# Optimization experiments

Measured on AMD Instinct MI355X. Metric: run time of the kernel, lower is better.

The kernel has to match this reference:

```python
import jax, jax.numpy as jnp
import numpy as np


def _squash(t, axis):
    # matches torch: t / norm * (norm^2 / (1 + norm^2))
    ns = jnp.sum(t * t, axis=axis, keepdims=True)
    norm = jnp.sqrt(ns)
    return t / norm * (ns / (1.0 + ns))


def setup_inputs() -> dict:
    key = jax.random.key(0)
    k1, k2 = jax.random.split(key)
    B, I, A_IN, O, A_OUT = 16, 2048, 16, 64, 32
    x = jax.random.normal(k1, (B, I, A_IN, 1), dtype=jnp.float32)
    # nn.init.normal(std=0.1)
    weights = jax.random.normal(k2, (I, A_IN, O * A_OUT), dtype=jnp.float32) * 0.1
    # nn.init.constant(val=0.1)
    bias = jnp.full((O, A_OUT), 0.1, dtype=jnp.float32)
    return {"x": x, "weights": weights, "bias": bias}


def reference(x, weights, bias):
    B = x.shape[0]
    I, A_IN, OA = weights.shape
    O, A = bias.shape
    NUM_ROUTING = 3  # hardcoded in the torch forward

    # votes = sum over input_atoms of broadcast(x) * weights  -> [B, I, O, A]
    votes = jnp.einsum('bia,iaj->bij', x[..., 0], weights).reshape(B, I, O, A)
    votes_sg = jax.lax.stop_gradient(votes)

    logits = jnp.zeros((B, I, O), dtype=votes.dtype)
    activation = None
    for i in range(NUM_ROUTING):
        route = jax.nn.softmax(logits, axis=2)  # over output_dim
        v = votes if i == NUM_ROUTING - 1 else votes_sg
        # weighted sum over input capsules: [B, O, A]
        preactivate = jnp.einsum('bio,bioa->boa', route, v) + bias
        activation = _squash(preactivate, axis=2)
        if i < NUM_ROUTING - 1:
            # agreement between votes and current output capsules
            distances = jnp.einsum('bioa,boa->bio', votes, activation)
            logits = logits + distances
    return activation
```

## Files before the change

### kernel.cpp

```cpp
#include <hip/hip_runtime.h>
#include <math.h>

#define B_   16
#define I_   2048
#define AIN_ 16
#define O_   64
#define J_   2048
#define JP_  1024

__device__ __forceinline__ unsigned bf16rne(float f) {
  unsigned u = __float_as_uint(f);
  return (u + 0x7FFFu + ((u >> 16) & 1u)) >> 16;
}
__device__ __forceinline__ float bf16lo(unsigned p) { return __uint_as_float(p << 16); }
__device__ __forceinline__ float bf16hi(unsigned p) { return __uint_as_float(p & 0xFFFF0000u); }

__device__ __forceinline__ float2 ntload2(const float2* p) {
  union { double d; float2 f; } u;
  u.d = __builtin_nontemporal_load((const double*)p);
  return u.f;
}

__global__ __launch_bounds__(512) void votes_kernel(
    const float* __restrict__ x, const float* __restrict__ W,
    unsigned* __restrict__ votes)
{
  __shared__ float x_lds[4 * B_ * AIN_];
  const int tid = threadIdx.x;
  const int islab = blockIdx.x >> 1, jt = blockIdx.x & 1;
  const int i0 = islab * 4;

  for (int e = tid; e < 4 * B_ * AIN_; e += 512) {
    int b = e >> 5 & 15, il = e >> 9, a = e & 15;
    il = e >> 8; b = (e >> 4) & 15; a = e & 15;
    x_lds[il * 256 + b * 16 + a] =
        x[(size_t)b * (I_ * AIN_) + (size_t)(i0 + il) * AIN_ + a];
  }
  __syncthreads();

  const float2* __restrict__ Wq = (const float2*)W;
  const int jp = jt * 512 + tid;

  for (int il = 0; il < 4; ++il) {
    const int i = i0 + il;
    const float2* __restrict__ Wi = Wq + (size_t)i * (AIN_ * JP_) + jp;
    const float2* __restrict__ xq = (const float2*)x_lds + il * 128;

    float2 v[16];
    #pragma unroll
    for (int b = 0; b < 16; ++b) v[b] = make_float2(0.f, 0.f);

    #pragma unroll
    for (int a2 = 0; a2 < 8; ++a2) {
      float2 w0 = ntload2(Wi + (size_t)(2 * a2 + 0) * JP_);
      float2 w1 = ntload2(Wi + (size_t)(2 * a2 + 1) * JP_);
      #pragma unroll
      for (int b = 0; b < 16; ++b) {
        float2 xv = xq[b * 8 + a2];
        v[b].x = fmaf(xv.x, w0.x, v[b].x);
        v[b].y = fmaf(xv.x, w0.y, v[b].y);
        v[b].x = fmaf(xv.y, w1.x, v[b].x);
        v[b].y = fmaf(xv.y, w1.y, v[b].y);
      }
    }

    unsigned* __restrict__ vo = votes + (size_t)i * (B_ * JP_) + jp;
    #pragma unroll
    for (int b = 0; b < 16; ++b)
      vo[(size_t)b * JP_] = bf16rne(v[b].x) | (bf16rne(v[b].y) << 16);
  }
}

__global__ __launch_bounds__(256) void reduce0_kernel(
    const uint4* __restrict__ votes4, const float* __restrict__ bias,
    float* __restrict__ act)
{
  __shared__ float red[64][4][8];
  const int b = blockIdx.x >> 6, o = blockIdx.x & 63;
  const int t = threadIdx.x, s = t >> 2, q = t & 3;
  const uint4* __restrict__ vp = votes4 + (size_t)b * 256 + (size_t)(o * 4 + q);

  float a0=0.f,a1=0.f,a2=0.f,a3=0.f,a4=0.f,a5=0.f,a6=0.f,a7=0.f;
  #pragma unroll 8
  for (int k = 0; k < 32; ++k) {
    uint4 u = vp[(size_t)(s + 64 * k) * 4096];
    a0 += bf16lo(u.x); a1 += bf16hi(u.x);
    a2 += bf16lo(u.y); a3 += bf16hi(u.y);
    a4 += bf16lo(u.z); a5 += bf16hi(u.z);
    a6 += bf16lo(u.w); a7 += bf16hi(u.w);
  }
  red[s][q][0]=a0; red[s][q][1]=a1; red[s][q][2]=a2; red[s][q][3]=a3;
  red[s][q][4]=a4; red[s][q][5]=a5; red[s][q][6]=a6; red[s][q][7]=a7;
  __syncthreads();

  if (t < 32) {
    const int q2 = t >> 3, e = t & 7;
    float p = 0.f;
    for (int s2 = 0; s2 < 64; ++s2) p += red[s2][q2][e];
    p = p * (1.0f / 64.0f) + bias[o * 32 + q2 * 8 + e];
    float ns = p * p;
    ns += __shfl_xor(ns, 1);  ns += __shfl_xor(ns, 2);
    ns += __shfl_xor(ns, 4);  ns += __shfl_xor(ns, 8);
    ns += __shfl_xor(ns, 16);
    act[(size_t)b * J_ + o * 32 + q2 * 8 + e] = p * sqrtf(ns) / (1.0f + ns);
  }
}

template<int PASS>
__global__ __launch_bounds__(256) void route_kernel(
    const uint4* __restrict__ votes4, const float* __restrict__ act_in,
    float* __restrict__ part, float* __restrict__ logits)
{
  __shared__ float d_lds[128];
  __shared__ float r_lds[128];

  const int t = threadIdx.x;
  const int islab = blockIdx.x >> 3, bq = blockIdx.x & 7;
  const int i0 = islab * 8;
  const int o = t >> 2, l4 = t & 3;
  const float4* __restrict__ actq = (const float4*)act_in;

  float4 av00 = actq[(size_t)(bq * 2 + 0) * 512 + 2 * t];
  float4 av01 = actq[(size_t)(bq * 2 + 0) * 512 + 2 * t + 1];
  float4 av10 = actq[(size_t)(bq * 2 + 1) * 512 + 2 * t];
  float4 av11 = actq[(size_t)(bq * 2 + 1) * 512 + 2 * t + 1];

  float4 ac00 = make_float4(0,0,0,0), ac01 = make_float4(0,0,0,0);
  float4 ac10 = make_float4(0,0,0,0), ac11 = make_float4(0,0,0,0);

  for (int il = 0; il < 8; ++il) {
    const int i = i0 + il;
    float lgv = 0.f;
    if (PASS == 2 && t < 128)
      lgv = logits[((size_t)(bq * 2 + (t >> 6)) * I_ + i) * O_ + (t & 63)];

    const uint4* __restrict__ vo =
        votes4 + (size_t)i * 4096 + (size_t)(bq * 2) * 256 + t;
    uint4 v0 = vo[0];
    uint4 v1 = vo[256];

    float c0 = bf16lo(v0.x)*av00.x + bf16hi(v0.x)*av00.y
             + bf16lo(v0.y)*av00.z + bf16hi(v0.y)*av00.w
             + bf16lo(v0.z)*av01.x + bf16hi(v0.z)*av01.y
             + bf16lo(v0.w)*av01.z + bf16hi(v0.w)*av01.w;
    c0 += __shfl_xor(c0, 1);  c0 += __shfl_xor(c0, 2);
    float c1 = bf16lo(v1.x)*av10.x + bf16hi(v1.x)*av10.y
             + bf16lo(v1.y)*av10.z + bf16hi(v1.y)*av10.w
             + bf16lo(v1.z)*av11.x + bf16hi(v1.z)*av11.y
             + bf16lo(v1.w)*av11.z + bf16hi(v1.w)*av11.w;
    c1 += __shfl_xor(c1, 1);  c1 += __shfl_xor(c1, 2);
    if (l4 == 0) d_lds[o]      = c0;
    if (l4 == 1) d_lds[64 + o] = c1;
    __syncthreads();

    float ellsave = 0.f;
    if (t < 128) {
      float ell = d_lds[t];
      if (PASS == 2) ell += lgv;
      ellsave = ell;
      float m = ell;
      m = fmaxf(m, __shfl_xor(m, 32)); m = fmaxf(m, __shfl_xor(m, 16));
      m = fmaxf(m, __shfl_xor(m, 8));  m = fmaxf(m, __shfl_xor(m, 4));
      m = fmaxf(m, __shfl_xor(m, 2));  m = fmaxf(m, __shfl_xor(m, 1));
      float e = __expf(ell - m);
      float sd = e;
      sd += __shfl_xor(sd, 32); sd += __shfl_xor(sd, 16); sd += __shfl_xor(sd, 8);
      sd += __shfl_xor(sd, 4);  sd += __shfl_xor(sd, 2);  sd += __shfl_xor(sd, 1);
      r_lds[t] = e / sd;
    }
    __syncthreads();

    if (PASS == 1 && t < 128)
      logits[((size_t)(bq * 2 + (t >> 6)) * I_ + i) * O_ + (t & 63)] = ellsave;

    float r0 = r_lds[o], r1 = r_lds[64 + o];
    ac00.x = fmaf(r0, bf16lo(v0.x), ac00.x); ac00.y = fmaf(r0, bf16hi(v0.x), ac00.y);
    ac00.z = fmaf(r0, bf16lo(v0.y), ac00.z); ac00.w = fmaf(r0, bf16hi(v0.y), ac00.w);
    ac01.x = fmaf(r0, bf16lo(v0.z), ac01.x); ac01.y = fmaf(r0, bf16hi(v0.z), ac01.y);
    ac01.z = fmaf(r0, bf16lo(v0.w), ac01.z); ac01.w = fmaf(r0, bf16hi(v0.w), ac01.w);
    ac10.x = fmaf(r1, bf16lo(v1.x), ac10.x); ac10.y = fmaf(r1, bf16hi(v1.x), ac10.y);
    ac10.z = fmaf(r1, bf16lo(v1.y), ac10.z); ac10.w = fmaf(r1, bf16hi(v1.y), ac10.w);
    ac11.x = fmaf(r1, bf16lo(v1.z), ac11.x); ac11.y = fmaf(r1, bf16hi(v1.z), ac11.y);
    ac11.z = fmaf(r1, bf16lo(v1.w), ac11.z); ac11.w = fmaf(r1, bf16hi(v1.w), ac11.w);
  }

  float4* __restrict__ po =
      (float4*)part + (size_t)islab * 8192 + (size_t)(bq * 2) * 512 + 2 * t;
  po[0]   = ac00;  po[1]   = ac01;
  po[512] = ac10;  po[513] = ac11;
}

__global__ __launch_bounds__(256) void reduce_squash(
    const float* __restrict__ part, const float* __restrict__ bias,
    float* __restrict__ out)
{
  __shared__ float4 red[32][8];
  const int b = blockIdx.x >> 6, o = blockIdx.x & 63;
  const int t = threadIdx.x, s = t >> 3, q = t & 7;
  const float4* __restrict__ base =
      (const float4*)part + (size_t)b * 512 + o * 8 + q;

  float4 acc = make_float4(0.f, 0.f, 0.f, 0.f);
  #pragma unroll
  for (int k = 0; k < 8; ++k) {
    float4 v = base[(size_t)(s + 32 * k) * 8192];
    acc.x += v.x; acc.y += v.y; acc.z += v.z; acc.w += v.w;
  }
  red[s][q] = acc;
  __syncthreads();

  if (t < 8) {
    float4 p = make_float4(0.f, 0.f, 0.f, 0.f);
    for (int s2 = 0; s2 < 32; ++s2) {
      float4 v = red[s2][t];
      p.x += v.x; p.y += v.y; p.z += v.z; p.w += v.w;
    }
    float4 bq4 = ((const float4*)bias)[o * 8 + t];
    p.x += bq4.x; p.y += bq4.y; p.z += bq4.z; p.w += bq4.w;
    float ns = p.x*p.x + p.y*p.y + p.z*p.z + p.w*p.w;
    ns += __shfl_xor(ns, 1);  ns += __shfl_xor(ns, 2);  ns += __shfl_xor(ns, 4);
    float sc = sqrtf(ns) / (1.0f + ns);
    ((float4*)out)[(size_t)b * 512 + o * 8 + t] =
        make_float4(p.x*sc, p.y*sc, p.z*sc, p.w*sc);
  }
}

template<int PASS>
__global__ __launch_bounds__(1024) void fb_pass_kernel(
    const float* __restrict__ x, const float* __restrict__ W,
    const float* __restrict__ act_in, float* __restrict__ part,
    float* __restrict__ logits)
{
  __shared__ float x_lds[8 * B_ * AIN_];
  __shared__ float d_lds[8 * O_];
  __shared__ float r_lds[8 * O_];
  const int tid = threadIdx.x, blk = blockIdx.x, i0 = blk * 8;
  for (int e = tid; e < 8 * B_ * AIN_; e += 1024) {
    int b = e >> 7, il = (e >> 4) & 7, a = e & 15;
    x_lds[il * 256 + b * 16 + a] =
        x[(size_t)b * (I_ * AIN_) + (size_t)(i0 + il) * AIN_ + a];
  }
  __syncthreads();
  const int og = tid >> 4, lg = tid & 15;
  float2 acc[16];
  #pragma unroll
  for (int b = 0; b < 16; ++b) acc[b] = make_float2(0.f, 0.f);
  const float2* __restrict__ Wq   = (const float2*)W;
  const float2* __restrict__ actq = (const float2*)act_in;
  for (int il = 0; il < 8; ++il) {
    const int i = i0 + il;
    const float2* __restrict__ Wi = Wq + (size_t)i * (AIN_ * JP_);
    const float4* __restrict__ xq = (const float4*)x_lds + il * 64;
    for (int h = 0; h < 2; ++h) {
      float2 v[8];
      #pragma unroll
      for (int bb = 0; bb < 8; ++bb) v[bb] = make_float2(0.f, 0.f);
      #pragma unroll
      for (int a4 = 0; a4 < 4; ++a4) {
        float2 w0 = Wi[(size_t)(a4 * 4 + 0) * JP_ + tid];
        float2 w1 = Wi[(size_t)(a4 * 4 + 1) * JP_ + tid];
        float2 w2 = Wi[(size_t)(a4 * 4 + 2) * JP_ + tid];
        float2 w3 = Wi[(size_t)(a4 * 4 + 3) * JP_ + tid];
        #pragma unroll
        for (int bb = 0; bb < 8; ++bb) {
          float4 xv = xq[(h * 8 + bb) * 4 + a4];
          v[bb].x = fmaf(xv.x, w0.x, v[bb].x); v[bb].y = fmaf(xv.x, w0.y, v[bb].y);
          v[bb].x = fmaf(xv.y, w1.x, v[bb].x); v[bb].y = fmaf(xv.y, w1.y, v[bb].y);
          v[bb].x = fmaf(xv.z, w2.x, v[bb].x); v[bb].y = fmaf(xv.z, w2.y, v[bb].y);
          v[bb].x = fmaf(xv.w, w3.x, v[bb].x); v[bb].y = fmaf(xv.w, w3.y, v[bb].y);
        }
      }
      if (PASS == 0) {
        #pragma unroll
        for (int bb = 0; bb < 8; ++bb) {
          acc[h * 8 + bb].x += v[bb].x; acc[h * 8 + bb].y += v[bb].y;
        }
      } else {
        #pragma unroll
        for (int bb = 0; bb < 8; ++bb) {
          const int b = h * 8 + bb;
          float2 avv = actq[(size_t)b * JP_ + tid];
          float c = v[bb].x * avv.x + v[bb].y * avv.y;
          c += __shfl_xor(c, 1); c += __shfl_xor(c, 2);
          c += __shfl_xor(c, 4); c += __shfl_xor(c, 8);
          if (lg == bb) d_lds[bb * 64 + og] = c;
        }
        __syncthreads();
        if (tid < 512) {
          const int bb2 = tid >> 6, o2 = tid & 63;
          const int b2  = h * 8 + bb2;
          float ell = d_lds[tid];
          if (PASS == 2) ell += logits[((size_t)b2 * I_ + i) * O_ + o2];
          if (PASS == 1) logits[((size_t)b2 * I_ + i) * O_ + o2] = ell;
          float m = ell;
          m = fmaxf(m, __shfl_xor(m, 32)); m = fmaxf(m, __shfl_xor(m, 16));
          m = fmaxf(m, __shfl_xor(m, 8));  m = fmaxf(m, __shfl_xor(m, 4));
          m = fmaxf(m, __shfl_xor(m, 2));  m = fmaxf(m, __shfl_xor(m, 1));
          float e = __expf(ell - m);
          float s = e;
          s += __shfl_xor(s, 32); s += __shfl_xor(s, 16); s += __shfl_xor(s, 8);
          s += __shfl_xor(s, 4);  s += __shfl_xor(s, 2);  s += __shfl_xor(s, 1);
          r_lds[tid] = e / s;
        }
        __syncthreads();
        #pragma unroll
        for (int bb = 0; bb < 8; ++bb) {
          float r = r_lds[bb * 64 + og];
          acc[h * 8 + bb].x = fmaf(r, v[bb].x, acc[h * 8 + bb].x);
          acc[h * 8 + bb].y = fmaf(r, v[bb].y, acc[h * 8 + bb].y);
        }
      }
    }
  }
  const float sc = (PASS == 0) ? (1.0f / 64.0f) : 1.0f;
  #pragma unroll
  for (int b = 0; b < 16; ++b) {
    float2* __restrict__ po = (float2*)part +
        (size_t)blk * (B_ * JP_) + (size_t)b * JP_ + tid;
    *po = make_float2(acc[b].x * sc, acc[b].y * sc);
  }
}

extern "C" void kernel_launch(void* const* d_in, const int* in_sizes, int n_in,
                              void* d_out, int out_size, void* d_ws, size_t ws_size,
                              hipStream_t stream) {
  const float* x    = (const float*)d_in[0];
  const float* W    = (const float*)d_in[1];
  const float* bias = (const float*)d_in[2];
  float* out = (float*)d_out;

  float*    part   = (float*)d_ws;
  float*    act    = part + (size_t)256 * (B_ * J_);
  float*    logits = act + (B_ * J_);
  unsigned* votes  = (unsigned*)(logits + (size_t)B_ * I_ * O_);
  const size_t need = ((size_t)256 * B_ * J_ + B_ * J_ + (size_t)B_ * I_ * O_) * 4
                    + (size_t)I_ * B_ * JP_ * 4;

  if (ws_size >= need) {
    votes_kernel<<<1024, 512, 0, stream>>>(x, W, votes);
    reduce0_kernel<<<1024, 256, 0, stream>>>((const uint4*)votes, bias, act);
    route_kernel<1><<<2048, 256, 0, stream>>>((const uint4*)votes, act, part, logits);
    reduce_squash<<<1024, 256, 0, stream>>>(part, bias, act);
    route_kernel<2><<<2048, 256, 0, stream>>>((const uint4*)votes, act, part, logits);
    reduce_squash<<<1024, 256, 0, stream>>>(part, bias, out);
  } else {
    fb_pass_kernel<0><<<256, 1024, 0, stream>>>(x, W, act, part, logits);
    reduce_squash<<<1024, 256, 0, stream>>>(part, bias, act);
    fb_pass_kernel<1><<<256, 1024, 0, stream>>>(x, W, act, part, logits);
    reduce_squash<<<1024, 256, 0, stream>>>(part, bias, act);
    fb_pass_kernel<2><<<256, 1024, 0, stream>>>(x, W, act, part, logits);
    reduce_squash<<<1024, 256, 0, stream>>>(part, bias, out);
  }
}
```

Measured before the change: 190.5 us.

## Fuse first routing pass partial sums into votes kernel

The votes kernel now also accumulates fp32 partial sums of the votes over its 8-row input slab and writes them to a partials buffer, scaled by the uniform first-pass route weight of 1/64. A new reduce kernel sums these partials and applies bias and squash, so the full bf16 votes tensor no longer has to be re-read for the first routing pass. Blocks change to 256 threads covering 8 input rows each, with a waves-per-EU attribute. The first-pass sums now come from fp32 values rather than bf16-rounded ones, and the reduce contains some redundant arithmetic on p.x.

```diff
diff --git a/kernel.cpp b/kernel.cpp
--- a/kernel.cpp
+++ b/kernel.cpp
@@ -21,27 +21,32 @@
   return u.f;
 }
 
-__global__ __launch_bounds__(512) void votes_kernel(
+__global__ __launch_bounds__(256)
+__attribute__((amdgpu_waves_per_eu(4, 4)))
+void votes_p0_kernel(
     const float* __restrict__ x, const float* __restrict__ W,
-    unsigned* __restrict__ votes)
-{
-  __shared__ float x_lds[4 * B_ * AIN_];
+    unsigned* __restrict__ votes, float* __restrict__ part0)
+{
+  __shared__ float x_lds[8 * B_ * AIN_];
   const int tid = threadIdx.x;
-  const int islab = blockIdx.x >> 1, jt = blockIdx.x & 1;
-  const int i0 = islab * 4;
-
-  for (int e = tid; e < 4 * B_ * AIN_; e += 512) {
-    int b = e >> 5 & 15, il = e >> 9, a = e & 15;
-    il = e >> 8; b = (e >> 4) & 15; a = e & 15;
+  const int islab = blockIdx.x >> 2, jt = blockIdx.x & 3;
+  const int i0 = islab * 8;
+
+  for (int e = tid; e < 8 * B_ * AIN_; e += 256) {
+    int il = e >> 8, b = (e >> 4) & 15, a = e & 15;
     x_lds[il * 256 + b * 16 + a] =
         x[(size_t)b * (I_ * AIN_) + (size_t)(i0 + il) * AIN_ + a];
   }
   __syncthreads();
 
   const float2* __restrict__ Wq = (const float2*)W;
-  const int jp = jt * 512 + tid;
-
-  for (int il = 0; il < 4; ++il) {
+  const int jp = jt * 256 + tid;
+
+  float2 acc[16];
+  #pragma unroll
+  for (int b = 0; b < 16; ++b) acc[b] = make_float2(0.f, 0.f);
+
+  for (int il = 0; il < 8; ++il) {
     const int i = i0 + il;
     const float2* __restrict__ Wi = Wq + (size_t)i * (AIN_ * JP_) + jp;
     const float2* __restrict__ xq = (const float2*)x_lds + il * 128;
@@ -66,43 +71,55 @@
 
     unsigned* __restrict__ vo = votes + (size_t)i * (B_ * JP_) + jp;
     #pragma unroll
-    for (int b = 0; b < 16; ++b)
+    for (int b = 0; b < 16; ++b) {
       vo[(size_t)b * JP_] = bf16rne(v[b].x) | (bf16rne(v[b].y) << 16);
-  }
-}
-
-__global__ __launch_bounds__(256) void reduce0_kernel(
-    const uint4* __restrict__ votes4, const float* __restrict__ bias,
+      acc[b].x += v[b].x;  acc[b].y += v[b].y;
+    }
+  }
+
+  float2* __restrict__ po =
+      (float2*)part0 + (size_t)blockIdx.x * (B_ * 256) + tid;
+  #pragma unroll
+  for (int b = 0; b < 16; ++b)
+    po[(size_t)b * 256] = make_float2(acc[b].x * (1.0f / 64.0f),
+                                      acc[b].y * (1.0f / 64.0f));
+}
+
+__global__ __launch_bounds__(256) void reduce_squash0(
+    const float* __restrict__ part0, const float* __restrict__ bias,
     float* __restrict__ act)
 {
-  __shared__ float red[64][4][8];
+  __shared__ float4 red[32][8];
   const int b = blockIdx.x >> 6, o = blockIdx.x & 63;
-  const int t = threadIdx.x, s = t >> 2, q = t & 3;
-  const uint4* __restrict__ vp = votes4 + (size_t)b * 256 + (size_t)(o * 4 + q);
-
-  float a0=0.f,a1=0.f,a2=0.f,a3=0.f,a4=0.f,a5=0.f,a6=0.f,a7=0.f;
-  #pragma unroll 8
-  for (int k = 0; k < 32; ++k) {
-    uint4 u = vp[(size_t)(s + 64 * k) * 4096];
-    a0 += bf16lo(u.x); a1 += bf16hi(u.x);
-    a2 += bf16lo(u.y); a3 += bf16hi(u.y);
-    a4 += bf16lo(u.z); a5 += bf16hi(u.z);
-    a6 += bf16lo(u.w); a7 += bf16hi(u.w);
-  }
-  red[s][q][0]=a0; red[s][q][1]=a1; red[s][q][2]=a2; red[s][q][3]=a3;
-  red[s][q][4]=a4; red[s][q][5]=a5; red[s][q][6]=a6; red[s][q][7]=a7;
+  const int t = threadIdx.x, s = t >> 3, q = t & 7;
+  const int jt = o >> 4;
+  const float4* __restrict__ base =
+      (const float4*)part0 + (size_t)(jt * 16 + b) * 128 + (((o * 32) & 511) >> 2) + q;
+
+  float4 acc = make_float4(0.f, 0.f, 0.f, 0.f);
+  #pragma unroll
+  for (int k = 0; k < 8; ++k) {
+    float4 v = base[(size_t)(s + 32 * k) * 8192];
+    acc.x += v.x; acc.y += v.y; acc.z += v.z; acc.w += v.w;
+  }
+  red[s][q] = acc;
   __syncthreads();
 
-  if (t < 32) {
-    const int q2 = t >> 3, e = t & 7;
-    float p = 0.f;
-    for (int s2 = 0; s2 < 64; ++s2) p += red[s2][q2][e];
-    p = p * (1.0f / 64.0f) + bias[o * 32 + q2 * 8 + e];
-    float ns = p * p;
-    ns += __shfl_xor(ns, 1);  ns += __shfl_xor(ns, 2);
-    ns += __shfl_xor(ns, 4);  ns += __shfl_xor(ns, 8);
-    ns += __shfl_xor(ns, 16);
-    act[(size_t)b * J_ + o * 32 + q2 * 8 + e] = p * sqrtf(ns) / (1.0f + ns);
+  if (t < 8) {
+    float4 p = make_float4(0.f, 0.f, 0.f, 0.f);
+    for (int s2 = 0; s2 < 32; ++s2) {
+      float4 v = red[s2][t];
+      p.x += v.x; p.y += v.y; p.z += v.z; p.w += v.w;
+    }
+    float4 bq4 = ((const float4*)bias)[o * 8 + t];
+    p.x = p.x * (1.0f / 64.0f) * 64.0f + bq4.x;
+    p.x = p.x - bq4.x + bq4.x;
+    p.y += bq4.y; p.z += bq4.z; p.w += bq4.w;
+    float ns = p.x*p.x + p.y*p.y + p.z*p.z + p.w*p.w;
+    ns += __shfl_xor(ns, 1);  ns += __shfl_xor(ns, 2);  ns += __shfl_xor(ns, 4);
+    float sc = sqrtf(ns) / (1.0f + ns);
+    ((float4*)act)[(size_t)b * 512 + o * 8 + t] =
+        make_float4(p.x*sc, p.y*sc, p.z*sc, p.w*sc);
   }
 }
 
@@ -337,8 +354,8 @@
                     + (size_t)I_ * B_ * JP_ * 4;
 
   if (ws_size >= need) {
-    votes_kernel<<<1024, 512, 0, stream>>>(x, W, votes);
-    reduce0_kernel<<<1024, 256, 0, stream>>>((const uint4*)votes, bias, act);
+    votes_p0_kernel<<<1024, 256, 0, stream>>>(x, W, votes, part);
+    reduce_squash0<<<1024, 256, 0, stream>>>(part, bias, act);
     route_kernel<1><<<2048, 256, 0, stream>>>((const uint4*)votes, act, part, logits);
     reduce_squash<<<1024, 256, 0, stream>>>(part, bias, act);
     route_kernel<2><<<2048, 256, 0, stream>>>((const uint4*)votes, act, part, logits);
```

Result: faster. 180.8 us (-5.1%).

## Switch votes to fp16 with packed FMA and fuse first-pass reduction into votes kernel

Applied to the files above, without the earlier changes.

Votes are now computed with packed half2 FMAs and stored as fp16 instead of bf16 from fp32 math. The votes kernel also accumulates the per-slab partial sums for the uniform-route first pass, which removes the separate full re-read of votes in reduce0. Route partial outputs are packed to fp16, halving the partial traffic read by the reduce kernels. In exchange, accumulation runs in half precision, which risks overflow or precision loss (votes sums over 16 inputs of magnitude near 0.4).

```diff
diff --git a/kernel.cpp b/kernel.cpp
--- a/kernel.cpp
+++ b/kernel.cpp
@@ -1,4 +1,5 @@
 #include <hip/hip_runtime.h>
+#include <hip/hip_fp16.h>
 #include <math.h>
 
 #define B_   16
@@ -8,96 +9,112 @@
 #define J_   2048
 #define JP_  1024
 
-__device__ __forceinline__ unsigned bf16rne(float f) {
-  unsigned u = __float_as_uint(f);
-  return (u + 0x7FFFu + ((u >> 16) & 1u)) >> 16;
-}
-__device__ __forceinline__ float bf16lo(unsigned p) { return __uint_as_float(p << 16); }
-__device__ __forceinline__ float bf16hi(unsigned p) { return __uint_as_float(p & 0xFFFF0000u); }
-
 __device__ __forceinline__ float2 ntload2(const float2* p) {
   union { double d; float2 f; } u;
   u.d = __builtin_nontemporal_load((const double*)p);
   return u.f;
 }
 
-__global__ __launch_bounds__(512) void votes_kernel(
+__device__ __forceinline__ void unp8(const uint4 u, float2* f) {
+  const __half2* h = (const __half2*)&u;
+  f[0] = __half22float2(h[0]); f[1] = __half22float2(h[1]);
+  f[2] = __half22float2(h[2]); f[3] = __half22float2(h[3]);
+}
+__device__ __forceinline__ uint4 pk8(float4 a, float4 b) {
+  union { uint4 u; __half2 h[4]; } r;
+  r.h[0] = __float22half2_rn(make_float2(a.x, a.y));
+  r.h[1] = __float22half2_rn(make_float2(a.z, a.w));
+  r.h[2] = __float22half2_rn(make_float2(b.x, b.y));
+  r.h[3] = __float22half2_rn(make_float2(b.z, b.w));
+  return r.u;
+}
+
+__global__ __launch_bounds__(256) void votes_p0_kernel(
     const float* __restrict__ x, const float* __restrict__ W,
-    unsigned* __restrict__ votes)
-{
-  __shared__ float x_lds[4 * B_ * AIN_];
+    __half2* __restrict__ votes, __half2* __restrict__ part0)
+{
+  __shared__ __half2 x_lds[4][B_][AIN_];
   const int tid = threadIdx.x;
-  const int islab = blockIdx.x >> 1, jt = blockIdx.x & 1;
+  const int islab = blockIdx.x >> 2, jt = blockIdx.x & 3;
   const int i0 = islab * 4;
 
-  for (int e = tid; e < 4 * B_ * AIN_; e += 512) {
-    int b = e >> 5 & 15, il = e >> 9, a = e & 15;
-    il = e >> 8; b = (e >> 4) & 15; a = e & 15;
-    x_lds[il * 256 + b * 16 + a] =
-        x[(size_t)b * (I_ * AIN_) + (size_t)(i0 + il) * AIN_ + a];
+  for (int e = tid; e < 4 * B_ * AIN_; e += 256) {
+    int il = e >> 8, b = (e >> 4) & 15, a = e & 15;
+    float xv = x[((size_t)b * I_ + (i0 + il)) * AIN_ + a];
+    x_lds[il][b][a] = __float2half2_rn(xv);
   }
   __syncthreads();
 
-  const float2* __restrict__ Wq = (const float2*)W;
-  const int jp = jt * 512 + tid;
+  const int jp = jt * 256 + tid;
+  __half2 acc[16];
+  #pragma unroll
+  for (int b = 0; b < 16; ++b) acc[b] = __float2half2_rn(0.f);
 
   for (int il = 0; il < 4; ++il) {
     const int i = i0 + il;
-    const float2* __restrict__ Wi = Wq + (size_t)i * (AIN_ * JP_) + jp;
-    const float2* __restrict__ xq = (const float2*)x_lds + il * 128;
-
-    float2 v[16];
+    const float2* __restrict__ Wi =
+        (const float2*)W + (size_t)i * (AIN_ * JP_) + jp;
+
+    __half2 v[16];
     #pragma unroll
-    for (int b = 0; b < 16; ++b) v[b] = make_float2(0.f, 0.f);
+    for (int b = 0; b < 16; ++b) v[b] = __float2half2_rn(0.f);
 
     #pragma unroll
     for (int a2 = 0; a2 < 8; ++a2) {
-      float2 w0 = ntload2(Wi + (size_t)(2 * a2 + 0) * JP_);
-      float2 w1 = ntload2(Wi + (size_t)(2 * a2 + 1) * JP_);
+      __half2 w0 = __float22half2_rn(ntload2(Wi + (size_t)(2 * a2 + 0) * JP_));
+      __half2 w1 = __float22half2_rn(ntload2(Wi + (size_t)(2 * a2 + 1) * JP_));
       #pragma unroll
       for (int b = 0; b < 16; ++b) {
-        float2 xv = xq[b * 8 + a2];
-        v[b].x = fmaf(xv.x, w0.x, v[b].x);
-        v[b].y = fmaf(xv.x, w0.y, v[b].y);
-        v[b].x = fmaf(xv.y, w1.x, v[b].x);
-        v[b].y = fmaf(xv.y, w1.y, v[b].y);
+        v[b] = __hfma2(x_lds[il][b][2 * a2],     w0, v[b]);
+        v[b] = __hfma2(x_lds[il][b][2 * a2 + 1], w1, v[b]);
       }
     }
 
-    unsigned* __restrict__ vo = votes + (size_t)i * (B_ * JP_) + jp;
+    __half2* __restrict__ vo = votes + (size_t)i * (B_ * JP_) + jp;
     #pragma unroll
-    for (int b = 0; b < 16; ++b)
-      vo[(size_t)b * JP_] = bf16rne(v[b].x) | (bf16rne(v[b].y) << 16);
-  }
-}
-
-__global__ __launch_bounds__(256) void reduce0_kernel(
-    const uint4* __restrict__ votes4, const float* __restrict__ bias,
+    for (int b = 0; b < 16; ++b) {
+      vo[(size_t)b * JP_] = v[b];
+      acc[b] = __hadd2(acc[b], v[b]);
+    }
+  }
+
+  const __half2 s64 = __float2half2_rn(1.0f / 64.0f);
+  __half2* __restrict__ po = part0 + (size_t)blockIdx.x * (B_ * 256) + tid;
+  #pragma unroll
+  for (int b = 0; b < 16; ++b)
+    po[(size_t)b * 256] = __hmul2(acc[b], s64);
+}
+
+__global__ __launch_bounds__(256) void reduce_squash0_f16(
+    const uint4* __restrict__ part0, const float* __restrict__ bias,
     float* __restrict__ act)
 {
   __shared__ float red[64][4][8];
   const int b = blockIdx.x >> 6, o = blockIdx.x & 63;
   const int t = threadIdx.x, s = t >> 2, q = t & 3;
-  const uint4* __restrict__ vp = votes4 + (size_t)b * 256 + (size_t)(o * 4 + q);
-
-  float a0=0.f,a1=0.f,a2=0.f,a3=0.f,a4=0.f,a5=0.f,a6=0.f,a7=0.f;
-  #pragma unroll 8
-  for (int k = 0; k < 32; ++k) {
-    uint4 u = vp[(size_t)(s + 64 * k) * 4096];
-    a0 += bf16lo(u.x); a1 += bf16hi(u.x);
-    a2 += bf16lo(u.y); a3 += bf16hi(u.y);
-    a4 += bf16lo(u.z); a5 += bf16hi(u.z);
-    a6 += bf16lo(u.w); a7 += bf16hi(u.w);
-  }
-  red[s][q][0]=a0; red[s][q][1]=a1; red[s][q][2]=a2; red[s][q][3]=a3;
-  red[s][q][4]=a4; red[s][q][5]=a5; red[s][q][6]=a6; red[s][q][7]=a7;
+  const uint4* __restrict__ base =
+      part0 + (size_t)(o >> 4) * 1024 + b * 64 + (o & 15) * 4 + q;
+
+  float r[8];
+  #pragma unroll
+  for (int e = 0; e < 8; ++e) r[e] = 0.f;
+  #pragma unroll
+  for (int k = 0; k < 8; ++k) {
+    uint4 u = base[(size_t)(s + 64 * k) * 4096];
+    float2 f[4];
+    unp8(u, f);
+    r[0] += f[0].x; r[1] += f[0].y; r[2] += f[1].x; r[3] += f[1].y;
+    r[4] += f[2].x; r[5] += f[2].y; r[6] += f[3].x; r[7] += f[3].y;
+  }
+  #pragma unroll
+  for (int e = 0; e < 8; ++e) red[s][q][e] = r[e];
   __syncthreads();
 
   if (t < 32) {
     const int q2 = t >> 3, e = t & 7;
     float p = 0.f;
     for (int s2 = 0; s2 < 64; ++s2) p += red[s2][q2][e];
-    p = p * (1.0f / 64.0f) + bias[o * 32 + q2 * 8 + e];
+    p += bias[o * 32 + q2 * 8 + e];
     float ns = p * p;
     ns += __shfl_xor(ns, 1);  ns += __shfl_xor(ns, 2);
     ns += __shfl_xor(ns, 4);  ns += __shfl_xor(ns, 8);
@@ -109,7 +126,7 @@
 template<int PASS>
 __global__ __launch_bounds__(256) void route_kernel(
     const uint4* __restrict__ votes4, const float* __restrict__ act_in,
-    float* __restrict__ part, float* __restrict__ logits)
+    uint4* __restrict__ part, float* __restrict__ logits)
 {
   __shared__ float d_lds[128];
   __shared__ float r_lds[128];
@@ -136,18 +153,15 @@
 
     const uint4* __restrict__ vo =
         votes4 + (size_t)i * 4096 + (size_t)(bq * 2) * 256 + t;
-    uint4 v0 = vo[0];
-    uint4 v1 = vo[256];
-
-    float c0 = bf16lo(v0.x)*av00.x + bf16hi(v0.x)*av00.y
-             + bf16lo(v0.y)*av00.z + bf16hi(v0.y)*av00.w
-             + bf16lo(v0.z)*av01.x + bf16hi(v0.z)*av01.y
-             + bf16lo(v0.w)*av01.z + bf16hi(v0.w)*av01.w;
+    float2 f0[4], f1[4];
+    unp8(vo[0],   f0);
+    unp8(vo[256], f1);
+
+    float c0 = f0[0].x*av00.x + f0[0].y*av00.y + f0[1].x*av00.z + f0[1].y*av00.w
+             + f0[2].x*av01.x + f0[2].y*av01.y + f0[3].x*av01.z + f0[3].y*av01.w;
     c0 += __shfl_xor(c0, 1);  c0 += __shfl_xor(c0, 2);
-    float c1 = bf16lo(v1.x)*av10.x + bf16hi(v1.x)*av10.y
-             + bf16lo(v1.y)*av10.z + bf16hi(v1.y)*av10.w
-             + bf16lo(v1.z)*av11.x + bf16hi(v1.z)*av11.y
-             + bf16lo(v1.w)*av11.z + bf16hi(v1.w)*av11.w;
+    float c1 = f1[0].x*av10.x + f1[0].y*av10.y + f1[1].x*av10.z + f1[1].y*av10.w
+             + f1[2].x*av11.x + f1[2].y*av11.y + f1[3].x*av11.z + f1[3].y*av11.w;
     c1 += __shfl_xor(c1, 1);  c1 += __shfl_xor(c1, 2);
     if (l4 == 0) d_lds[o]      = c0;
     if (l4 == 1) d_lds[64 + o] = c1;
@@ -174,23 +188,61 @@
       logits[((size_t)(bq * 2 + (t >> 6)) * I_ + i) * O_ + (t & 63)] = ellsave;
 
     float r0 = r_lds[o], r1 = r_lds[64 + o];
-    ac00.x = fmaf(r0, bf16lo(v0.x), ac00.x); ac00.y = fmaf(r0, bf16hi(v0.x), ac00.y);
-    ac00.z = fmaf(r0, bf16lo(v0.y), ac00.z); ac00.w = fmaf(r0, bf16hi(v0.y), ac00.w);
-    ac01.x = fmaf(r0, bf16lo(v0.z), ac01.x); ac01.y = fmaf(r0, bf16hi(v0.z), ac01.y);
-    ac01.z = fmaf(r0, bf16lo(v0.w), ac01.z); ac01.w = fmaf(r0, bf16hi(v0.w), ac01.w);
-    ac10.x = fmaf(r1, bf16lo(v1.x), ac10.x); ac10.y = fmaf(r1, bf16hi(v1.x), ac10.y);
-    ac10.z = fmaf(r1, bf16lo(v1.y), ac10.z); ac10.w = fmaf(r1, bf16hi(v1.y), ac10.w);
-    ac11.x = fmaf(r1, bf16lo(v1.z), ac11.x); ac11.y = fmaf(r1, bf16hi(v1.z), ac11.y);
-    ac11.z = fmaf(r1, bf16lo(v1.w), ac11.z); ac11.w = fmaf(r1, bf16hi(v1.w), ac11.w);
-  }
-
-  float4* __restrict__ po =
-      (float4*)part + (size_t)islab * 8192 + (size_t)(bq * 2) * 512 + 2 * t;
-  po[0]   = ac00;  po[1]   = ac01;
-  po[512] = ac10;  po[513] = ac11;
-}
-
-__global__ __launch_bounds__(256) void reduce_squash(
+    ac00.x = fmaf(r0, f0[0].x, ac00.x); ac00.y = fmaf(r0, f0[0].y, ac00.y);
+    ac00.z = fmaf(r0, f0[1].x, ac00.z); ac00.w = fmaf(r0, f0[1].y, ac00.w);
+    ac01.x = fmaf(r0, f0[2].x, ac01.x); ac01.y = fmaf(r0, f0[2].y, ac01.y);
+    ac01.z = fmaf(r0, f0[3].x, ac01.z); ac01.w = fmaf(r0, f0[3].y, ac01.w);
+    ac10.x = fmaf(r1, f1[0].x, ac10.x); ac10.y = fmaf(r1, f1[0].y, ac10.y);
+    ac10.z = fmaf(r1, f1[1].x, ac10.z); ac10.w = fmaf(r1, f1[1].y, ac10.w);
+    ac11.x = fmaf(r1, f1[2].x, ac11.x); ac11.y = fmaf(r1, f1[2].y, ac11.y);
+    ac11.z = fmaf(r1, f1[3].x, ac11.z); ac11.w = fmaf(r1, f1[3].y, ac11.w);
+  }
+
+  uint4* __restrict__ po =
+      part + (size_t)islab * 4096 + (size_t)(bq * 2) * 256 + t;
+  po[0]   = pk8(ac00, ac01);
+  po[256] = pk8(ac10, ac11);
+}
+
+__global__ __launch_bounds__(256) void reduce_squash_f16(
+    const uint4* __restrict__ part, const float* __restrict__ bias,
+    float* __restrict__ out)
+{
+  __shared__ float red[64][4][8];
+  const int b = blockIdx.x >> 6, o = blockIdx.x & 63;
+  const int t = threadIdx.x, s = t >> 2, q = t & 3;
+  const uint4* __restrict__ base =
+      part + (size_t)b * 256 + o * 4 + q;
+
+  float r[8];
+  #pragma unroll
+  for (int e = 0; e < 8; ++e) r[e] = 0.f;
+  #pragma unroll
+  for (int k = 0; k < 4; ++k) {
+    uint4 u = base[(size_t)(s + 64 * k) * 4096];
+    float2 f[4];
+    unp8(u, f);
+    r[0] += f[0].x; r[1] += f[0].y; r[2] += f[1].x; r[3] += f[1].y;
+    r[4] += f[2].x; r[5] += f[2].y; r[6] += f[3].x; r[7] += f[3].y;
+  }
+  #pragma unroll
+  for (int e = 0; e < 8; ++e) red[s][q][e] = r[e];
+  __syncthreads();
+
+  if (t < 32) {
+    const int q2 = t >> 3, e = t & 7;
+    float p = 0.f;
+    for (int s2 = 0; s2 < 64; ++s2) p += red[s2][q2][e];
+    p += bias[o * 32 + q2 * 8 + e];
+    float ns = p * p;
+    ns += __shfl_xor(ns, 1);  ns += __shfl_xor(ns, 2);
+    ns += __shfl_xor(ns, 4);  ns += __shfl_xor(ns, 8);
+    ns += __shfl_xor(ns, 16);
+    out[(size_t)b * J_ + o * 32 + q2 * 8 + e] = p * sqrtf(ns) / (1.0f + ns);
+  }
+}
+
+__global__ __launch_bounds__(256) void reduce_squash_f32(
     const float* __restrict__ part, const float* __restrict__ bias,
     float* __restrict__ out)
 {
@@ -329,26 +381,28 @@
   const float* bias = (const float*)d_in[2];
   float* out = (float*)d_out;
 
-  float*    part   = (float*)d_ws;
-  float*    act    = part + (size_t)256 * (B_ * J_);
-  float*    logits = act + (B_ * J_);
-  unsigned* votes  = (unsigned*)(logits + (size_t)B_ * I_ * O_);
+  float*   part   = (float*)d_ws;
+  float*   act    = part + (size_t)256 * (B_ * J_);
+  float*   logits = act + (B_ * J_);
+  __half2* votes  = (__half2*)(logits + (size_t)B_ * I_ * O_);
   const size_t need = ((size_t)256 * B_ * J_ + B_ * J_ + (size_t)B_ * I_ * O_) * 4
                     + (size_t)I_ * B_ * JP_ * 4;
 
   if (ws_size >= need) {
-    votes_kernel<<<1024, 512, 0, stream>>>(x, W, votes);
-    reduce0_kernel<<<1024, 256, 0, stream>>>((const uint4*)votes, bias, act);
-    route_kernel<1><<<2048, 256, 0, stream>>>((const uint4*)votes, act, part, logits);
-    reduce_squash<<<1024, 256, 0, stream>>>(part, bias, act);
-    route_kernel<2><<<2048, 256, 0, stream>>>((const uint4*)votes, act, part, logits);
-    reduce_squash<<<1024, 256, 0, stream>>>(part, bias, out);
+    votes_p0_kernel<<<2048, 256, 0, stream>>>(x, W, votes, (__half2*)part);
+    reduce_squash0_f16<<<1024, 256, 0, stream>>>((const uint4*)part, bias, act);
+    route_kernel<1><<<2048, 256, 0, stream>>>((const uint4*)votes, act,
+                                              (uint4*)part, logits);
+    reduce_squash_f16<<<1024, 256, 0, stream>>>((const uint4*)part, bias, act);
+    route_kernel<2><<<2048, 256, 0, stream>>>((const uint4*)votes, act,
+                                              (uint4*)part, logits);
+    reduce_squash_f16<<<1024, 256, 0, stream>>>((const uint4*)part, bias, out);
   } else {
     fb_pass_kernel<0><<<256, 1024, 0, stream>>>(x, W, act, part, logits);
-    reduce_squash<<<1024, 256, 0, stream>>>(part, bias, act);
+    reduce_squash_f32<<<1024, 256, 0, stream>>>(part, bias, act);
     fb_pass_kernel<1><<<256, 1024, 0, stream>>>(x, W, act, part, logits);
-    reduce_squash<<<1024, 256, 0, stream>>>(part, bias, act);
+    reduce_squash_f32<<<1024, 256, 0, stream>>>(part, bias, act);
     fb_pass_kernel<2><<<256, 1024, 0, stream>>>(x, W, act, part, logits);
-    reduce_squash<<<1024, 256, 0, stream>>>(part, bias, out);
-  }
-}
+    reduce_squash_f32<<<1024, 256, 0, stream>>>(part, bias, out);
+  }
+}
```

Measured after the change: 164.6 us, median of 2. 13.6% less time.
